# Optimization experiments

Measured on AMD Instinct MI355X. Metric: run time of the kernel, lower is better.

## Reference

```python
import jax, jax.numpy as jnp
import numpy as np

N, M, DIM, OUT_DIM = 50000, 512, 256, 256
NEG = -1e9


def setup_inputs() -> dict:
    key = jax.random.key(0)
    k1, k2, k3, k4, k5, k6 = jax.random.split(key, 6)
    node_features = jax.random.normal(k1, (N, DIM), dtype=jnp.float32)
    # each node assigned to one molecule (sorted segment ids)
    mol_ids = jnp.sort(jax.random.randint(k2, (N,), 0, M))
    mol_node_matrix = (mol_ids[None, :] == jnp.arange(M)[:, None]).astype(jnp.float32)  # [M, N]
    mol_node_mask = jnp.where(mol_node_matrix > 0, 0.0, NEG).astype(jnp.float32)  # [M, N]
    # Linear params (PyTorch-style uniform init)
    bound = 1.0 / np.sqrt(DIM)
    W_attend = jax.random.uniform(k3, (DIM, OUT_DIM), minval=-bound, maxval=bound, dtype=jnp.float32)
    b_attend = jax.random.uniform(k4, (OUT_DIM,), minval=-bound, maxval=bound, dtype=jnp.float32)
    w_align = jax.random.uniform(k5, (DIM, 1), minval=-bound, maxval=bound, dtype=jnp.float32)
    b_align = jax.random.uniform(k6, (1,), minval=-bound, maxval=bound, dtype=jnp.float32)
    return {"node_features": node_features, "mol_node_matrix": mol_node_matrix,
            "mol_node_mask": mol_node_mask, "W_attend": W_attend, "b_attend": b_attend,
            "w_align": w_align, "b_align": b_align}


def reference(node_features, mol_node_matrix, mol_node_mask, W_attend, b_attend, w_align, b_align):
    # h = LeakyReLU(attend(x)) : [N, out_dim]
    h = jax.nn.leaky_relu(node_features @ W_attend + b_attend, negative_slope=0.01)
    # a = align(x) : [N]  (dropout p=0 -> identity)
    a = (node_features @ w_align + b_align)[:, 0]
    # mol_node_matrix @ diag(a) == mol_node_matrix * a[None, :]  (same math, no NxN diag)
    logits = mol_node_matrix * a[None, :] + mol_node_mask  # [M, N]
    mol_node_weight = jax.nn.softmax(logits, axis=1)
    return mol_node_weight @ h, mol_node_weight
```

## Files before the change

### kernel.cpp

```cpp
#include <hip/hip_runtime.h>
#include <cstdint>
#include <cstddef>

#define N_NODES 50000
#define M_MOLS  512
#define DIMK    256
#define ODIM    256

#define NCH   99
#define CW    32
#define NSAMP (NCH * CW)

#define NB_SAMP  NCH
#define NB_WPACK 32
#define K1_GRID  (NB_SAMP + NB_WPACK)

#define K2T   512
#define A_CAP 4096
#define NF4   (N_NODES / 4)

typedef float  f32x4  __attribute__((ext_vector_type(4)));
typedef __bf16 bf16x8 __attribute__((ext_vector_type(8)));

static __device__ __forceinline__ short f2bf(float f) {
  unsigned u = __builtin_bit_cast(unsigned, f);
  u = u + 0x7fffu + ((u >> 16) & 1u);
  return (short)(u >> 16);
}

static __device__ __forceinline__ int chunk_base(int c) {
  return (c < NCH - 1) ? c * 512 : (N_NODES - CW);
}
static __device__ __forceinline__ int scol(int idx) {
  return chunk_base(idx >> 5) + (idx & 31);
}

__global__ __launch_bounds__(256) void k_prep(
    const float* __restrict__ mat, const float* __restrict__ W,
    int* __restrict__ smolid, int4* __restrict__ wp) {
  int b = blockIdx.x, t = threadIdx.x;
  if (b < NB_SAMP) {
    int base = chunk_base(b);
    int cp = (t & 15) * 2;
    int rg = t >> 4;
    int idx = -1, idy = -1;
    const float* p0 = mat + (size_t)(rg * 32) * N_NODES + base + cp;
#pragma unroll 16
    for (int r = 0; r < 32; r++) {
      float2 v = *(const float2*)(p0 + (size_t)r * N_NODES);
      if (v.x != 0.f) idx = rg * 32 + r;
      if (v.y != 0.f) idy = rg * 32 + r;
    }
    __shared__ int sm[16][32];
    sm[rg][cp] = idx; sm[rg][cp + 1] = idy;
    __syncthreads();
    if (t < 32) {
      int best = -1;
#pragma unroll
      for (int g = 0; g < 16; g++) best = max(best, sm[g][t]);
      smolid[b * CW + t] = best;
    }
  } else {
    int g  = (b - NB_SAMP) * 256 + t;
    int l  = g & 63;
    int Ju = g >> 6;
    int J  = Ju >> 3, u = Ju & 7;
    int j  = J * 16 + (l & 15);
    int k0 = u * 32 + (l >> 4) * 8;
    short sv[8];
#pragma unroll
    for (int i = 0; i < 8; i++) sv[i] = f2bf(W[(size_t)(k0 + i) * ODIM + j]);
    wp[Ju * 64 + l] = *(int4*)sv;
  }
}

__global__ __launch_bounds__(K2T, 2) void k_main(
    const float* __restrict__ x, const float* __restrict__ mat,
    const float* __restrict__ wa, const float* __restrict__ ba,
    const int* __restrict__ smolid, const int4* __restrict__ wp,
    const float* __restrict__ bias, float* __restrict__ out0,
    float* __restrict__ out1) {
  int m = blockIdx.x;
  int t = threadIdx.x;

  __shared__ float a_lds[A_CAP];
  __shared__ __align__(16) short xs[16 * 256];
  __shared__ float fred[8];
  __shared__ int   ired[8];
  __shared__ int   sseg[2];

  for (int which = 0; which < 2; which++) {
    int mm = m + which;
    int lo = 0, hi = NSAMP;
    while (lo < hi) { int mid = (lo + hi) >> 1; if (smolid[mid] < mm) lo = mid + 1; else hi = mid; }
    int res;
    if (lo == 0) res = 0;
    else if (lo >= NSAMP) res = N_NODES;
    else {
      int chi = scol(lo), clo = scol(lo - 1);
      if (chi == clo + 1) res = chi;
      else {
        int bh = smolid[lo];
        res = -1;
        for (int r = mm; r <= bh; r++) {
          int f = 0x7fffffff;
          int col = clo + 1 + t;
          if (col <= chi && mat[(size_t)r * N_NODES + col] != 0.f) f = col;
#pragma unroll
          for (int o = 1; o < 64; o <<= 1) f = min(f, __shfl_xor(f, o));
          if ((t & 63) == 0) ired[t >> 6] = f;
          __syncthreads();
          int gmin = ired[0];
#pragma unroll
          for (int i = 1; i < 8; i++) gmin = min(gmin, ired[i]);
          __syncthreads();
          if (gmin != 0x7fffffff) { res = gmin; break; }
        }
        if (res < 0) res = chi;
      }
    }
    if (t == 0) sseg[which] = res;
  }
  __syncthreads();
  int seg_s = sseg[0], seg_e = sseg[1];
  int L = seg_e - seg_s;

  int s4 = seg_s >> 2, e4 = (seg_e + 3) >> 2;
  float4* orow = (float4*)out1 + (size_t)m * NF4;
  float4 zz; zz.x = zz.y = zz.z = zz.w = 0.f;
  for (int q = t; q < NF4; q += K2T)
    if (q < s4 || q >= e4) orow[q] = zz;

  float ba0 = ba[0];
  int sub = t & 7;
  float4 wv[8];
  {
    const float4* wr = (const float4*)wa + sub * 8;
#pragma unroll
    for (int i = 0; i < 8; i++) wv[i] = wr[i];
  }
  int nit = (L + 63) >> 6;
  for (int it = 0; it < nit; it++) {
    int ro  = it * 64 + (t >> 3);
    int row = seg_s + ro;
    float s = 0.f;
    if (row < seg_e) {
      const float4* xr = (const float4*)(x + (size_t)row * DIMK) + sub * 8;
#pragma unroll
      for (int i = 0; i < 8; i++) {
        float4 xv = xr[i];
        s += xv.x * wv[i].x + xv.y * wv[i].y + xv.z * wv[i].z + xv.w * wv[i].w;
      }
    }
    s += __shfl_xor(s, 1); s += __shfl_xor(s, 2); s += __shfl_xor(s, 4);
    if (sub == 0 && row < seg_e && ro < A_CAP) a_lds[ro] = s + ba0;
  }
  __syncthreads();

  float mx = -3e38f;
  for (int i = t; i < L; i += K2T) mx = fmaxf(mx, a_lds[i]);
#pragma unroll
  for (int o = 1; o < 64; o <<= 1) mx = fmaxf(mx, __shfl_xor(mx, o));
  if ((t & 63) == 0) fred[t >> 6] = mx;
  __syncthreads();
  mx = fred[0];
#pragma unroll
  for (int i = 1; i < 8; i++) mx = fmaxf(mx, fred[i]);
  __syncthreads();
  float sm = 0.f;
  for (int i = t; i < L; i += K2T) sm += __expf(a_lds[i] - mx);
#pragma unroll
  for (int o = 1; o < 64; o <<= 1) sm += __shfl_xor(sm, o);
  if ((t & 63) == 0) fred[t >> 6] = sm;
  __syncthreads();
  sm = 0.f;
#pragma unroll
  for (int i = 0; i < 8; i++) sm += fred[i];
  float inv = (sm > 0.f) ? 1.f / sm : 0.f;
  for (int i = t; i < L; i += K2T) a_lds[i] = __expf(a_lds[i] - mx) * inv;
  __syncthreads();

  for (int q = s4 + t; q < e4; q += K2T) {
    int n = q * 4;
    float4 o;
    o.x = (n     >= seg_s && n     < seg_e) ? a_lds[n     - seg_s] : 0.f;
    o.y = (n + 1 >= seg_s && n + 1 < seg_e) ? a_lds[n + 1 - seg_s] : 0.f;
    o.z = (n + 2 >= seg_s && n + 2 < seg_e) ? a_lds[n + 2 - seg_s] : 0.f;
    o.w = (n + 3 >= seg_s && n + 3 < seg_e) ? a_lds[n + 3 - seg_s] : 0.f;
    orow[q] = o;
  }

  int wv_id = t >> 6, l = t & 63;
  bf16x8 wfrag[2][8];
#pragma unroll
  for (int t2 = 0; t2 < 2; t2++)
#pragma unroll
    for (int u = 0; u < 8; u++)
      wfrag[t2][u] = __builtin_bit_cast(bf16x8, wp[((wv_id * 2 + t2) * 8 + u) * 64 + l]);
  float bias_r[2];
#pragma unroll
  for (int t2 = 0; t2 < 2; t2++) bias_r[t2] = bias[wv_id * 32 + t2 * 16 + (l & 15)];

  float pooled[2] = {0.f, 0.f};
  int r = l & 15, g = l >> 4;
  int swr = (r & 7) << 4;

  int srow = t >> 5;
  int c0b  = (t & 31) * 16;
  int ssw  = (srow & 7) << 4;
  char* lb = (char*)xs;

  int nt2 = (L + 15) >> 4;
  for (int tile = 0; tile < nt2; tile++) {
    int base = seg_s + tile * 16;
    __syncthreads();
    {
      int n = base + srow;
      short sv[8];
      if (n < seg_e) {
        const float4* src = (const float4*)(x + (size_t)n * DIMK) + (t & 31) * 2;
        float4 A = src[0], B = src[1];
        sv[0] = f2bf(A.x); sv[1] = f2bf(A.y); sv[2] = f2bf(A.z); sv[3] = f2bf(A.w);
        sv[4] = f2bf(B.x); sv[5] = f2bf(B.y); sv[6] = f2bf(B.z); sv[7] = f2bf(B.w);
      } else {
#pragma unroll
        for (int i = 0; i < 8; i++) sv[i] = 0;
      }
      *(int4*)(lb + (srow << 9) + (c0b ^ ssw)) = *(int4*)sv;
    }
    __syncthreads();
    bf16x8 af[8];
#pragma unroll
    for (int u = 0; u < 8; u++)
      af[u] = __builtin_bit_cast(bf16x8,
                *(const int4*)(lb + (r << 9) + (((u << 6) + (g << 4)) ^ swr)));
#pragma unroll
    for (int t2 = 0; t2 < 2; t2++) {
      f32x4 acc = {0.f, 0.f, 0.f, 0.f};
#pragma unroll
      for (int u = 0; u < 8; u++)
        acc = __builtin_amdgcn_mfma_f32_16x16x32_bf16(af[u], wfrag[t2][u], acc, 0, 0, 0);
      float p = 0.f;
#pragma unroll
      for (int i = 0; i < 4; i++) {
        int ridx = tile * 16 + (g << 2) + i;
        float wgt = (ridx < L) ? a_lds[ridx] : 0.f;
        float h = acc[i] + bias_r[t2];
        h = h > 0.f ? h : 0.01f * h;
        p += wgt * h;
      }
      pooled[t2] += p;
    }
  }
#pragma unroll
  for (int t2 = 0; t2 < 2; t2++) {
    float p = pooled[t2];
    p += __shfl_xor(p, 16);
    p += __shfl_xor(p, 32);
    pooled[t2] = p;
  }
  if (l < 16) {
#pragma unroll
    for (int t2 = 0; t2 < 2; t2++)
      out0[m * ODIM + wv_id * 32 + t2 * 16 + l] = pooled[t2];
  }
}

extern "C" void kernel_launch(void* const* d_in, const int* in_sizes, int n_in,
                              void* d_out, int out_size, void* d_ws, size_t ws_size,
                              hipStream_t stream) {
  const float* x   = (const float*)d_in[0];
  const float* mat = (const float*)d_in[1];
  const float* W   = (const float*)d_in[3];
  const float* bA  = (const float*)d_in[4];
  const float* wa  = (const float*)d_in[5];
  const float* ba  = (const float*)d_in[6];

  float* out0 = (float*)d_out;
  float* out1 = out0 + (size_t)M_MOLS * ODIM;

  char* ws     = (char*)d_ws;
  int*  smolid = (int*) (ws);
  int4* wp     = (int4*)(ws + 16384);

  k_prep<<<K1_GRID, 256, 0, stream>>>(mat, W, smolid, wp);
  k_main<<<M_MOLS, K2T, 0, stream>>>(x, mat, wa, ba, smolid, wp, bA, out0, out1);
}
```

Measured before the change: 48.34 us.

## Split main kernel into align, segment-softmax, and interleaved pool/write kernels

The per-molecule main kernel becomes three stages. The align dot product now runs over all nodes in the prep kernel, a new per-molecule kernel finds segment bounds and writes normalized softmax weights to global memory, and the final kernel interleaves pooling blocks with many small dense-write blocks that fill the large [M,N] weight matrix, 8 rows per block. This spreads the dominant 100MB output write across many more blocks for better bandwidth, and removes the per-molecule serial align pass and the LDS cap on segment length. It costs an extra kernel launch and a round trip through global memory for the align values and weights.

New measurement: 79.20 us. 63.8% more time.

```diff
diff --git a/kernel.cpp b/kernel.cpp
--- a/kernel.cpp
+++ b/kernel.cpp
@@ -13,10 +13,14 @@
 
 #define NB_SAMP  NCH
 #define NB_WPACK 32
-#define K1_GRID  (NB_SAMP + NB_WPACK)
-
-#define K2T   512
-#define A_CAP 4096
+#define NB_ALIGN 1563
+#define K1_GRID  (NB_SAMP + NB_WPACK + NB_ALIGN)
+
+#define POOL_BLOCKS 512
+#define WCOLS 25
+#define WROWS 8
+#define NB_WRITE (WCOLS * (M_MOLS / WROWS))
+#define K3_GRID (POOL_BLOCKS + NB_WRITE)
 #define NF4   (N_NODES / 4)
 
 typedef float  f32x4  __attribute__((ext_vector_type(4)));
@@ -36,8 +40,10 @@
 }
 
 __global__ __launch_bounds__(256) void k_prep(
-    const float* __restrict__ mat, const float* __restrict__ W,
-    int* __restrict__ smolid, int4* __restrict__ wp) {
+    const float* __restrict__ x, const float* __restrict__ mat,
+    const float* __restrict__ W, const float* __restrict__ wa,
+    const float* __restrict__ ba,
+    float* __restrict__ a, int* __restrict__ smolid, int4* __restrict__ wp) {
   int b = blockIdx.x, t = threadIdx.x;
   if (b < NB_SAMP) {
     int base = chunk_base(b);
@@ -60,7 +66,7 @@
       for (int g = 0; g < 16; g++) best = max(best, sm[g][t]);
       smolid[b * CW + t] = best;
     }
-  } else {
+  } else if (b < NB_SAMP + NB_WPACK) {
     int g  = (b - NB_SAMP) * 256 + t;
     int l  = g & 63;
     int Ju = g >> 6;
@@ -71,22 +77,30 @@
 #pragma unroll
     for (int i = 0; i < 8; i++) sv[i] = f2bf(W[(size_t)(k0 + i) * ODIM + j]);
     wp[Ju * 64 + l] = *(int4*)sv;
-  }
-}
-
-__global__ __launch_bounds__(K2T, 2) void k_main(
-    const float* __restrict__ x, const float* __restrict__ mat,
-    const float* __restrict__ wa, const float* __restrict__ ba,
-    const int* __restrict__ smolid, const int4* __restrict__ wp,
-    const float* __restrict__ bias, float* __restrict__ out0,
-    float* __restrict__ out1) {
-  int m = blockIdx.x;
-  int t = threadIdx.x;
-
-  __shared__ float a_lds[A_CAP];
-  __shared__ __align__(16) short xs[16 * 256];
-  __shared__ float fred[8];
-  __shared__ int   ired[8];
+  } else {
+    int tid = (b - NB_SAMP - NB_WPACK) * 256 + t;
+    int row = tid >> 3, sub = tid & 7;
+    if (row >= N_NODES) return;
+    const float4* xr = (const float4*)(x + (size_t)row * DIMK) + sub * 8;
+    const float4* wr = (const float4*)wa + sub * 8;
+    float s = 0.f;
+#pragma unroll
+    for (int i = 0; i < 8; i++) {
+      float4 xv = xr[i], wv = wr[i];
+      s += xv.x * wv.x + xv.y * wv.y + xv.z * wv.z + xv.w * wv.w;
+    }
+    s += __shfl_xor(s, 1); s += __shfl_xor(s, 2); s += __shfl_xor(s, 4);
+    if (sub == 0) a[row] = s + ba[0];
+  }
+}
+
+__global__ __launch_bounds__(256) void k_bstats(
+    const float* __restrict__ a, const float* __restrict__ mat,
+    const int* __restrict__ smolid, int* __restrict__ strt,
+    float* __restrict__ wval) {
+  int m = blockIdx.x, t = threadIdx.x;
+  __shared__ float fred[4];
+  __shared__ int   ired[4];
   __shared__ int   sseg[2];
 
   for (int which = 0; which < 2; which++) {
@@ -101,18 +115,20 @@
       if (chi == clo + 1) res = chi;
       else {
         int bh = smolid[lo];
+        int Wd = chi - clo;
         res = -1;
         for (int r = mm; r <= bh; r++) {
+          const float* rp = mat + (size_t)r * N_NODES;
           int f = 0x7fffffff;
-          int col = clo + 1 + t;
-          if (col <= chi && mat[(size_t)r * N_NODES + col] != 0.f) f = col;
+          for (int i = t; i < Wd; i += 256) {
+            int col = clo + 1 + i;
+            if (rp[col] != 0.f) { f = col; break; }
+          }
 #pragma unroll
           for (int o = 1; o < 64; o <<= 1) f = min(f, __shfl_xor(f, o));
           if ((t & 63) == 0) ired[t >> 6] = f;
           __syncthreads();
-          int gmin = ired[0];
-#pragma unroll
-          for (int i = 1; i < 8; i++) gmin = min(gmin, ired[i]);
+          int gmin = min(min(ired[0], ired[1]), min(ired[2], ired[3]));
           __syncthreads();
           if (gmin != 0x7fffffff) { res = gmin; break; }
         }
@@ -122,75 +138,70 @@
     if (t == 0) sseg[which] = res;
   }
   __syncthreads();
-  int seg_s = sseg[0], seg_e = sseg[1];
-  int L = seg_e - seg_s;
-
-  int s4 = seg_s >> 2, e4 = (seg_e + 3) >> 2;
-  float4* orow = (float4*)out1 + (size_t)m * NF4;
-  float4 zz; zz.x = zz.y = zz.z = zz.w = 0.f;
-  for (int q = t; q < NF4; q += K2T)
-    if (q < s4 || q >= e4) orow[q] = zz;
-
-  float ba0 = ba[0];
-  int sub = t & 7;
-  float4 wv[8];
-  {
-    const float4* wr = (const float4*)wa + sub * 8;
-#pragma unroll
-    for (int i = 0; i < 8; i++) wv[i] = wr[i];
-  }
-  int nit = (L + 63) >> 6;
-  for (int it = 0; it < nit; it++) {
-    int ro  = it * 64 + (t >> 3);
-    int row = seg_s + ro;
-    float s = 0.f;
-    if (row < seg_e) {
-      const float4* xr = (const float4*)(x + (size_t)row * DIMK) + sub * 8;
-#pragma unroll
-      for (int i = 0; i < 8; i++) {
-        float4 xv = xr[i];
-        s += xv.x * wv[i].x + xv.y * wv[i].y + xv.z * wv[i].z + xv.w * wv[i].w;
-      }
-    }
-    s += __shfl_xor(s, 1); s += __shfl_xor(s, 2); s += __shfl_xor(s, 4);
-    if (sub == 0 && row < seg_e && ro < A_CAP) a_lds[ro] = s + ba0;
-  }
-  __syncthreads();
+  int s = sseg[0], e = sseg[1];
+  if (t == 0) {
+    strt[m] = s;
+    if (m == M_MOLS - 1) strt[M_MOLS] = e;
+  }
 
   float mx = -3e38f;
-  for (int i = t; i < L; i += K2T) mx = fmaxf(mx, a_lds[i]);
+  for (int i = s + t; i < e; i += 256) mx = fmaxf(mx, a[i]);
 #pragma unroll
   for (int o = 1; o < 64; o <<= 1) mx = fmaxf(mx, __shfl_xor(mx, o));
   if ((t & 63) == 0) fred[t >> 6] = mx;
   __syncthreads();
-  mx = fred[0];
-#pragma unroll
-  for (int i = 1; i < 8; i++) mx = fmaxf(mx, fred[i]);
+  mx = fmaxf(fmaxf(fred[0], fred[1]), fmaxf(fred[2], fred[3]));
   __syncthreads();
   float sm = 0.f;
-  for (int i = t; i < L; i += K2T) sm += __expf(a_lds[i] - mx);
+  for (int i = s + t; i < e; i += 256) sm += __expf(a[i] - mx);
 #pragma unroll
   for (int o = 1; o < 64; o <<= 1) sm += __shfl_xor(sm, o);
   if ((t & 63) == 0) fred[t >> 6] = sm;
   __syncthreads();
-  sm = 0.f;
-#pragma unroll
-  for (int i = 0; i < 8; i++) sm += fred[i];
+  sm = fred[0] + fred[1] + fred[2] + fred[3];
   float inv = (sm > 0.f) ? 1.f / sm : 0.f;
-  for (int i = t; i < L; i += K2T) a_lds[i] = __expf(a_lds[i] - mx) * inv;
-  __syncthreads();
-
-  for (int q = s4 + t; q < e4; q += K2T) {
-    int n = q * 4;
-    float4 o;
-    o.x = (n     >= seg_s && n     < seg_e) ? a_lds[n     - seg_s] : 0.f;
-    o.y = (n + 1 >= seg_s && n + 1 < seg_e) ? a_lds[n + 1 - seg_s] : 0.f;
-    o.z = (n + 2 >= seg_s && n + 2 < seg_e) ? a_lds[n + 2 - seg_s] : 0.f;
-    o.w = (n + 3 >= seg_s && n + 3 < seg_e) ? a_lds[n + 3 - seg_s] : 0.f;
-    orow[q] = o;
-  }
-
+  for (int i = s + t; i < e; i += 256) wval[i] = __expf(a[i] - mx) * inv;
+}
+
+__global__ __launch_bounds__(512, 4) void k_out(
+    const float* __restrict__ x, const float* __restrict__ wval,
+    const int* __restrict__ strt, const int4* __restrict__ wp,
+    const float* __restrict__ bias, float* __restrict__ out0,
+    float* __restrict__ out1) {
+  int b  = blockIdx.x;
+  int pb = b >> 2;
+  bool isPool = ((b & 3) == 0) && (pb < POOL_BLOCKS);
+  int t = threadIdx.x;
+
+  if (!isPool) {
+    int before = (pb < POOL_BLOCKS) ? (pb + 1) : POOL_BLOCKS;
+    int wb = b - before;
+    int mc = wb / WCOLS;
+    int c  = wb % WCOLS;
+    int n4 = c * 512 + t;
+    if (n4 >= NF4) return;
+    int n = n4 * 4;
+    float4 w = *(const float4*)(wval + n);
+    int m0 = mc * WROWS;
+#pragma unroll
+    for (int r = 0; r < WROWS; r++) {
+      int m = m0 + r;
+      int s = strt[m], e = strt[m + 1];
+      float4 o;
+      o.x = ((unsigned)(n     - s) < (unsigned)(e - s)) ? w.x : 0.f;
+      o.y = ((unsigned)(n + 1 - s) < (unsigned)(e - s)) ? w.y : 0.f;
+      o.z = ((unsigned)(n + 2 - s) < (unsigned)(e - s)) ? w.z : 0.f;
+      o.w = ((unsigned)(n + 3 - s) < (unsigned)(e - s)) ? w.w : 0.f;
+      *(float4*)(out1 + (size_t)m * N_NODES + n) = o;
+    }
+    return;
+  }
+
+  int m = pb;
+  int seg_s = strt[m], seg_e = strt[m + 1];
+  int L = seg_e - seg_s;
   int wv_id = t >> 6, l = t & 63;
+
   bf16x8 wfrag[2][8];
 #pragma unroll
   for (int t2 = 0; t2 < 2; t2++)
@@ -204,6 +215,9 @@
   float pooled[2] = {0.f, 0.f};
   int r = l & 15, g = l >> 4;
   int swr = (r & 7) << 4;
+
+  __shared__ __align__(16) short xs[16 * 256];
+  __shared__ float wt[16];
 
   int srow = t >> 5;
   int c0b  = (t & 31) * 16;
@@ -227,6 +241,10 @@
         for (int i = 0; i < 8; i++) sv[i] = 0;
       }
       *(int4*)(lb + (srow << 9) + (c0b ^ ssw)) = *(int4*)sv;
+      if (t < 16) {
+        int nn = base + t;
+        wt[t] = (nn < seg_e) ? wval[nn] : 0.f;
+      }
     }
     __syncthreads();
     bf16x8 af[8];
@@ -243,11 +261,9 @@
       float p = 0.f;
 #pragma unroll
       for (int i = 0; i < 4; i++) {
-        int ridx = tile * 16 + (g << 2) + i;
-        float wgt = (ridx < L) ? a_lds[ridx] : 0.f;
         float h = acc[i] + bias_r[t2];
         h = h > 0.f ? h : 0.01f * h;
-        p += wgt * h;
+        p += wt[(g << 2) + i] * h;
       }
       pooled[t2] += p;
     }
@@ -279,10 +295,14 @@
   float* out0 = (float*)d_out;
   float* out1 = out0 + (size_t)M_MOLS * ODIM;
 
-  char* ws     = (char*)d_ws;
-  int*  smolid = (int*) (ws);
-  int4* wp     = (int4*)(ws + 16384);
-
-  k_prep<<<K1_GRID, 256, 0, stream>>>(mat, W, smolid, wp);
-  k_main<<<M_MOLS, K2T, 0, stream>>>(x, mat, wa, ba, smolid, wp, bA, out0, out1);
-}
+  char*  ws     = (char*)d_ws;
+  float* a      = (float*)(ws);
+  int*   smolid = (int*)  (ws + 200064);
+  int*   strt   = (int*)  (ws + 212800);
+  float* wval   = (float*)(ws + 214912);
+  int4*  wp     = (int4*) (ws + 414912);
+
+  k_prep  <<<K1_GRID, 256, 0, stream>>>(x, mat, W, wa, ba, a, smolid, wp);
+  k_bstats<<<M_MOLS, 256, 0, stream>>>(a, mat, smolid, strt, wval);
+  k_out   <<<K3_GRID, 512, 0, stream>>>(x, wval, strt, wp, bA, out0, out1);
+}
```

## Precompute segment bounds in separate kernel and split zero-fill across extra blocks

Applied to the files above, without the earlier changes.

Segment start computation moves out of the main kernel into a new bounds kernel. That kernel scans the gaps between sampled columns once per gap instead of doing a per-molecule binary search plus row scans. The main kernel launches three blocks per molecule: two stream nontemporal zero stores over halves of the weight row, and one does the attention and pooling. It also cuts the a_lds capacity to 1024 and raises the occupancy hint. The cost is an extra kernel launch, and segments longer than 1024 nodes would overflow the reduced capacity, which the random test data is unlikely to hit.

Result: slower. 56.79 us (+17.5%).

```diff
diff --git a/kernel.cpp b/kernel.cpp
--- a/kernel.cpp
+++ b/kernel.cpp
@@ -10,14 +10,14 @@
 #define NCH   99
 #define CW    32
 #define NSAMP (NCH * CW)
-
-#define NB_SAMP  NCH
+#define NGAP  (NCH - 1)
+
 #define NB_WPACK 32
-#define K1_GRID  (NB_SAMP + NB_WPACK)
-
-#define K2T   512
-#define A_CAP 4096
+#define B2_GRID  (NGAP + NCH + 1 + NB_WPACK)
+
 #define NF4   (N_NODES / 4)
+#define HALF4 6250
+#define A_CAP 1024
 
 typedef float  f32x4  __attribute__((ext_vector_type(4)));
 typedef __bf16 bf16x8 __attribute__((ext_vector_type(8)));
@@ -31,37 +31,79 @@
 static __device__ __forceinline__ int chunk_base(int c) {
   return (c < NCH - 1) ? c * 512 : (N_NODES - CW);
 }
-static __device__ __forceinline__ int scol(int idx) {
-  return chunk_base(idx >> 5) + (idx & 31);
-}
-
-__global__ __launch_bounds__(256) void k_prep(
+
+__global__ __launch_bounds__(256) void k_samp(
+    const float* __restrict__ mat, int* __restrict__ smolid) {
+  int b = blockIdx.x, t = threadIdx.x;
+  int base = chunk_base(b);
+  int cp = (t & 15) * 2;
+  int rg = t >> 4;
+  int idx = -1, idy = -1;
+  const float* p0 = mat + (size_t)(rg * 32) * N_NODES + base + cp;
+#pragma unroll 16
+  for (int r = 0; r < 32; r++) {
+    float2 v = *(const float2*)(p0 + (size_t)r * N_NODES);
+    if (v.x != 0.f) idx = rg * 32 + r;
+    if (v.y != 0.f) idy = rg * 32 + r;
+  }
+  __shared__ int sm[16][32];
+  sm[rg][cp] = idx; sm[rg][cp + 1] = idy;
+  __syncthreads();
+  if (t < 32) {
+    int best = -1;
+#pragma unroll
+    for (int g = 0; g < 16; g++) best = max(best, sm[g][t]);
+    smolid[b * CW + t] = best;
+  }
+}
+
+__global__ __launch_bounds__(256) void k_bounds(
     const float* __restrict__ mat, const float* __restrict__ W,
-    int* __restrict__ smolid, int4* __restrict__ wp) {
+    const int* __restrict__ smolid, int* __restrict__ strt,
+    int4* __restrict__ wp) {
   int b = blockIdx.x, t = threadIdx.x;
-  if (b < NB_SAMP) {
-    int base = chunk_base(b);
-    int cp = (t & 15) * 2;
-    int rg = t >> 4;
-    int idx = -1, idy = -1;
-    const float* p0 = mat + (size_t)(rg * 32) * N_NODES + base + cp;
-#pragma unroll 16
-    for (int r = 0; r < 32; r++) {
-      float2 v = *(const float2*)(p0 + (size_t)r * N_NODES);
-      if (v.x != 0.f) idx = rg * 32 + r;
-      if (v.y != 0.f) idy = rg * 32 + r;
-    }
-    __shared__ int sm[16][32];
-    sm[rg][cp] = idx; sm[rg][cp + 1] = idy;
+  if (b < NGAP) {
+    int p  = chunk_base(b) + CW - 1;
+    int q  = chunk_base(b + 1);
+    int ag = smolid[b * CW + CW - 1];
+    int bg = smolid[(b + 1) * CW];
+    if (bg == ag) return;
+    int Wd = q - p;
+    int nr = bg - ag;
+    __shared__ int f1[512];
+    int wave = t >> 6, l = t & 63;
+    for (int rr = wave; rr < nr; rr += 4) {
+      const float* rp = mat + (size_t)(ag + 1 + rr) * N_NODES + p + 1;
+      int mn = 0x7fffffff;
+      for (int i = l; i < Wd; i += 64)
+        if (rp[i] != 0.f) { mn = i; break; }
+#pragma unroll
+      for (int o = 1; o < 64; o <<= 1) mn = min(mn, __shfl_xor(mn, o));
+      if (l == 0) f1[rr] = mn;
+    }
     __syncthreads();
-    if (t < 32) {
-      int best = -1;
-#pragma unroll
-      for (int g = 0; g < 16; g++) best = max(best, sm[g][t]);
-      smolid[b * CW + t] = best;
+    if (t == 0) {
+      int run = 0x7fffffff;
+      for (int rr = nr - 1; rr >= 0; rr--) {
+        run = min(run, f1[rr]);
+        strt[ag + 1 + rr] = p + 1 + run;
+      }
+    }
+  } else if (b < NGAP + NCH) {
+    int cc = b - NGAP;
+    if (t >= 1 && t < CW) {
+      int prev = smolid[cc * CW + t - 1], cur = smolid[cc * CW + t];
+      int col = chunk_base(cc) + t;
+      for (int m = prev + 1; m <= cur; m++) strt[m] = col;
+    }
+  } else if (b == NGAP + NCH) {
+    int first = smolid[0], last = smolid[NSAMP - 1];
+    for (int m = t; m <= M_MOLS; m += 256) {
+      if (m <= first) strt[m] = 0;
+      else if (m > last) strt[m] = N_NODES;
     }
   } else {
-    int g  = (b - NB_SAMP) * 256 + t;
+    int g  = (b - NGAP - NCH - 1) * 256 + t;
     int l  = g & 63;
     int Ju = g >> 6;
     int J  = Ju >> 3, u = Ju & 7;
@@ -74,62 +116,31 @@
   }
 }
 
-__global__ __launch_bounds__(K2T, 2) void k_main(
-    const float* __restrict__ x, const float* __restrict__ mat,
-    const float* __restrict__ wa, const float* __restrict__ ba,
-    const int* __restrict__ smolid, const int4* __restrict__ wp,
-    const float* __restrict__ bias, float* __restrict__ out0,
-    float* __restrict__ out1) {
-  int m = blockIdx.x;
+__global__ __launch_bounds__(512, 4) void k_fused(
+    const float* __restrict__ x, const float* __restrict__ wa,
+    const float* __restrict__ ba, const int* __restrict__ strt,
+    const int4* __restrict__ wp, const float* __restrict__ bias,
+    float* __restrict__ out0, float* __restrict__ out1) {
+  int b = blockIdx.x;
+  int m = b / 3, role = b - m * 3;
   int t = threadIdx.x;
-
+  int seg_s = strt[m], seg_e = strt[m + 1];
+
+  if (role != 0) {
+    int s4 = seg_s >> 2, e4 = (seg_e + 3) >> 2;
+    f32x4* orow = (f32x4*)out1 + (size_t)m * NF4;
+    f32x4 z = {0.f, 0.f, 0.f, 0.f};
+    int q0 = (role - 1) * HALF4;
+    int q1 = q0 + HALF4;
+    for (int q = q0 + t; q < q1; q += 512)
+      if (q < s4 || q >= e4) __builtin_nontemporal_store(z, orow + q);
+    return;
+  }
+
+  int L = seg_e - seg_s;
   __shared__ float a_lds[A_CAP];
   __shared__ __align__(16) short xs[16 * 256];
   __shared__ float fred[8];
-  __shared__ int   ired[8];
-  __shared__ int   sseg[2];
-
-  for (int which = 0; which < 2; which++) {
-    int mm = m + which;
-    int lo = 0, hi = NSAMP;
-    while (lo < hi) { int mid = (lo + hi) >> 1; if (smolid[mid] < mm) lo = mid + 1; else hi = mid; }
-    int res;
-    if (lo == 0) res = 0;
-    else if (lo >= NSAMP) res = N_NODES;
-    else {
-      int chi = scol(lo), clo = scol(lo - 1);
-      if (chi == clo + 1) res = chi;
-      else {
-        int bh = smolid[lo];
-        res = -1;
-        for (int r = mm; r <= bh; r++) {
-          int f = 0x7fffffff;
-          int col = clo + 1 + t;
-          if (col <= chi && mat[(size_t)r * N_NODES + col] != 0.f) f = col;
-#pragma unroll
-          for (int o = 1; o < 64; o <<= 1) f = min(f, __shfl_xor(f, o));
-          if ((t & 63) == 0) ired[t >> 6] = f;
-          __syncthreads();
-          int gmin = ired[0];
-#pragma unroll
-          for (int i = 1; i < 8; i++) gmin = min(gmin, ired[i]);
-          __syncthreads();
-          if (gmin != 0x7fffffff) { res = gmin; break; }
-        }
-        if (res < 0) res = chi;
-      }
-    }
-    if (t == 0) sseg[which] = res;
-  }
-  __syncthreads();
-  int seg_s = sseg[0], seg_e = sseg[1];
-  int L = seg_e - seg_s;
-
-  int s4 = seg_s >> 2, e4 = (seg_e + 3) >> 2;
-  float4* orow = (float4*)out1 + (size_t)m * NF4;
-  float4 zz; zz.x = zz.y = zz.z = zz.w = 0.f;
-  for (int q = t; q < NF4; q += K2T)
-    if (q < s4 || q >= e4) orow[q] = zz;
 
   float ba0 = ba[0];
   int sub = t & 7;
@@ -158,7 +169,7 @@
   __syncthreads();
 
   float mx = -3e38f;
-  for (int i = t; i < L; i += K2T) mx = fmaxf(mx, a_lds[i]);
+  for (int i = t; i < L; i += 512) mx = fmaxf(mx, a_lds[i]);
 #pragma unroll
   for (int o = 1; o < 64; o <<= 1) mx = fmaxf(mx, __shfl_xor(mx, o));
   if ((t & 63) == 0) fred[t >> 6] = mx;
@@ -168,7 +179,7 @@
   for (int i = 1; i < 8; i++) mx = fmaxf(mx, fred[i]);
   __syncthreads();
   float sm = 0.f;
-  for (int i = t; i < L; i += K2T) sm += __expf(a_lds[i] - mx);
+  for (int i = t; i < L; i += 512) sm += __expf(a_lds[i] - mx);
 #pragma unroll
   for (int o = 1; o < 64; o <<= 1) sm += __shfl_xor(sm, o);
   if ((t & 63) == 0) fred[t >> 6] = sm;
@@ -177,17 +188,21 @@
 #pragma unroll
   for (int i = 0; i < 8; i++) sm += fred[i];
   float inv = (sm > 0.f) ? 1.f / sm : 0.f;
-  for (int i = t; i < L; i += K2T) a_lds[i] = __expf(a_lds[i] - mx) * inv;
-  __syncthreads();
-
-  for (int q = s4 + t; q < e4; q += K2T) {
-    int n = q * 4;
-    float4 o;
-    o.x = (n     >= seg_s && n     < seg_e) ? a_lds[n     - seg_s] : 0.f;
-    o.y = (n + 1 >= seg_s && n + 1 < seg_e) ? a_lds[n + 1 - seg_s] : 0.f;
-    o.z = (n + 2 >= seg_s && n + 2 < seg_e) ? a_lds[n + 2 - seg_s] : 0.f;
-    o.w = (n + 3 >= seg_s && n + 3 < seg_e) ? a_lds[n + 3 - seg_s] : 0.f;
-    orow[q] = o;
+  for (int i = t; i < L; i += 512) a_lds[i] = __expf(a_lds[i] - mx) * inv;
+  __syncthreads();
+
+  {
+    int s4 = seg_s >> 2, e4 = (seg_e + 3) >> 2;
+    float4* orow = (float4*)out1 + (size_t)m * NF4;
+    for (int q = s4 + t; q < e4; q += 512) {
+      int n = q * 4;
+      float4 o;
+      o.x = (n     >= seg_s && n     < seg_e) ? a_lds[n     - seg_s] : 0.f;
+      o.y = (n + 1 >= seg_s && n + 1 < seg_e) ? a_lds[n + 1 - seg_s] : 0.f;
+      o.z = (n + 2 >= seg_s && n + 2 < seg_e) ? a_lds[n + 2 - seg_s] : 0.f;
+      o.w = (n + 3 >= seg_s && n + 3 < seg_e) ? a_lds[n + 3 - seg_s] : 0.f;
+      orow[q] = o;
+    }
   }
 
   int wv_id = t >> 6, l = t & 63;
@@ -281,8 +296,10 @@
 
   char* ws     = (char*)d_ws;
   int*  smolid = (int*) (ws);
-  int4* wp     = (int4*)(ws + 16384);
-
-  k_prep<<<K1_GRID, 256, 0, stream>>>(mat, W, smolid, wp);
-  k_main<<<M_MOLS, K2T, 0, stream>>>(x, mat, wa, ba, smolid, wp, bA, out0, out1);
-}
+  int*  strt   = (int*) (ws + 16384);
+  int4* wp     = (int4*)(ws + 20480);
+
+  k_samp  <<<NCH, 256, 0, stream>>>(mat, smolid);
+  k_bounds<<<B2_GRID, 256, 0, stream>>>(mat, W, smolid, strt, wp);
+  k_fused <<<M_MOLS * 3, 512, 0, stream>>>(x, wa, ba, strt, wp, bA, out0, out1);
+}
```
